# Optimization experiments

Measured on AMD Instinct MI355X. Metric: run time of the kernel, lower is better.

## Reference

```python
import jax, jax.numpy as jnp
import numpy as np
import math

D_MODEL = 1024
N_HEADS = 16
C = 1
B, L = 8, 2048


def _glorot(key, fan):
    lim = np.sqrt(6.0 / (fan + fan)).astype(np.float32)
    return jax.random.uniform(key, (fan, fan), jnp.float32, -lim, lim)


def setup_inputs() -> dict:
    key = jax.random.key(0)
    ks = jax.random.split(key, 7)
    queries = jax.random.normal(ks[0], (B, L, D_MODEL), jnp.float32)
    keys = jax.random.normal(ks[1], (B, L, D_MODEL), jnp.float32)
    values = jax.random.normal(ks[2], (B, L, D_MODEL), jnp.float32)
    wq = _glorot(ks[3], D_MODEL)
    wk = _glorot(ks[4], D_MODEL)
    wv = _glorot(ks[5], D_MODEL)
    wo = _glorot(ks[6], D_MODEL)
    return {"queries": queries, "keys": keys, "values": values,
            "wq": wq, "wk": wk, "wv": wv, "wo": wo}


def reference(queries, keys, values, wq, wk, wv, wo):
    Bv, Lv, _ = queries.shape
    H = N_HEADS
    Dh = D_MODEL // N_HEADS
    # Projections, then (B, L, H, Dh) -> (B, H, Dh, L)  (time axis last)
    Q = (queries @ wq).reshape(Bv, Lv, H, Dh).transpose(0, 2, 3, 1)
    K = (keys @ wk).reshape(Bv, Lv, H, Dh).transpose(0, 2, 3, 1)
    V = (values @ wv).reshape(Bv, Lv, H, Dh).transpose(0, 2, 3, 1)
    # FFT-based autocorrelation over the time axis, per (B,H,Dh) lane
    corr = jnp.fft.irfft(jnp.fft.rfft(Q, axis=-1) * jnp.conj(jnp.fft.rfft(K, axis=-1)), n=Lv, axis=-1)  # (B,H,Dh,L)
    k_top = int(math.floor(C * math.log(Lv)))
    top_vals, top_idx = jax.lax.top_k(corr, k_top)          # (B,H,Dh,k)
    w = jax.nn.softmax(top_vals, axis=-1)                    # (B,H,Dh,k)
    # Faithful to original roll_function: it rolls along the Dh axis
    # (which the source mislabels as seq_len), shifts taken mod Dh.
    # out[b,h,t,:] = V[b,h,(t - tau[b,h,t]) % Dh, :]
    t = jnp.arange(Dh)
    out = jnp.zeros_like(V)
    for i in range(k_top):  # small static loop (k_top = 7)
        gather_idx = (t[None, None, :] - top_idx[..., i]) % Dh   # (B,H,Dh)
        rolled = jnp.take_along_axis(V, gather_idx[..., None], axis=2)  # (B,H,Dh,L)
        out = out + w[..., i, None] * rolled
    # Faithful layout-scrambling reshape: (B,H,Dh,L)->(B,Dh,H,L)->(B,L,d_model)
    out = out.transpose(0, 2, 1, 3).reshape(Bv, Lv, D_MODEL)
    return out @ wo
```

## Files before the change

kernel.cpp:

```cpp
#include <hip/hip_runtime.h>
#include <math.h>

#define NB 8
#define NL 2048
#define ND 1024
#define NH 16
#define KTOP 7

typedef __attribute__((ext_vector_type(4))) float f32x4;
typedef __attribute__((ext_vector_type(8))) short s16x8;
typedef __attribute__((ext_vector_type(8))) _Float16 f16x8;
typedef __attribute__((ext_vector_type(4))) _Float16 f16x4;

__device__ __forceinline__ unsigned short f2bf(float x) {
  unsigned u = __float_as_uint(x);
  u = (u + 0x7FFFu + ((u >> 16) & 1u)) >> 16;
  return (unsigned short)u;
}
__device__ __forceinline__ float bf2f(unsigned short h) {
  return __uint_as_float(((unsigned)h) << 16);
}
__device__ __forceinline__ unsigned cvtpk_bf16(float a, float b) {
  unsigned d;
  asm("v_cvt_pk_bf16_f32 %0, %1, %2" : "=v"(d) : "v"(a), "v"(b));
  return d;
}
__device__ __forceinline__ float lo16(unsigned h) { return __uint_as_float(h << 16); }
__device__ __forceinline__ float hi16(unsigned h) { return __uint_as_float(h & 0xffff0000u); }

__device__ __forceinline__ void gll16(const void* g, void* l) {
  __builtin_amdgcn_global_load_lds(
      (const __attribute__((address_space(1))) void*)g,
      (__attribute__((address_space(3))) void*)l, 16, 0, 0);
}

__global__ __launch_bounds__(256) void wprep_kernel(
    const float* __restrict__ w0, const float* __restrict__ w1,
    const float* __restrict__ w2, const float* __restrict__ w3,
    short* __restrict__ wsplit, _Float16* __restrict__ wf16) {
  __shared__ float tile[32][33];
  int y = blockIdx.y;
  const float* in = (y == 0) ? w0 : (y == 1) ? w1 : (y == 2) ? w2 : w3;
  int bx = blockIdx.x & 31, by = blockIdx.x >> 5;
  int tx = threadIdx.x & 31, ty = threadIdx.x >> 5;
#pragma unroll
  for (int i = 0; i < 4; ++i)
    tile[ty + i * 8][tx] = in[(size_t)(by * 32 + ty + i * 8) * ND + bx * 32 + tx];
  __syncthreads();
#pragma unroll
  for (int i = 0; i < 4; ++i) {
    float x = tile[tx][ty + i * 8];
    int n = bx * 32 + ty + i * 8;
    int k = by * 32 + tx;
    if (y < 2) {
      short* oh = wsplit + (size_t)(2 * y) * ND * ND;
      short* ol = wsplit + (size_t)(2 * y + 1) * ND * ND;
      unsigned short h = f2bf(x);
      unsigned short l = f2bf(x - bf2f(h));
      size_t o = (size_t)n * ND + (k ^ ((n & 3) << 3));
      oh[o] = (short)h;
      ol[o] = (short)l;
    } else {
      _Float16* of = wf16 + (size_t)(y - 2) * ND * ND;
      of[(size_t)n * ND + (k ^ ((n & 7) << 3))] = (_Float16)x;
    }
  }
}

__global__ __launch_bounds__(256) void gemm_split(
    const float* __restrict__ A, const short* __restrict__ BhT,
    const short* __restrict__ BlT, float* __restrict__ Ct) {
  constexpr int K = 1024;
  __shared__ short ah[4096], al[4096], bh[4096], bl[4096];
  int t = threadIdx.x;
  int wg = (blockIdx.x & 7) * 128 + (blockIdx.x >> 3);
  int m0 = (wg >> 3) << 7, n0 = (wg & 7) << 7;
  int lane = t & 63;
  int wm = (t >> 7) & 1, wn = (t >> 6) & 1;
  int lrow = lane & 15, lk8 = (lane >> 4) << 3;

  f32x4 acc[4][4] = {};

  for (int k0 = 0; k0 < K; k0 += 32) {
#pragma unroll
    for (int it = 0; it < 2; ++it) {
      int cb = it * 256 + t;
      int r = cb >> 2, c8 = (cb & 3) << 3;
      int lo = it * 2048 + (t & 192) * 8;
      gll16(BhT + (size_t)(n0 + r) * K + k0 + c8, bh + lo);
      gll16(BlT + (size_t)(n0 + r) * K + k0 + c8, bl + lo);
    }
#pragma unroll
    for (int it = 0; it < 2; ++it) {
      int ca = it * 256 + t;
      int r = ca >> 2, c8 = (ca & 3) << 3;
      const float* pa = A + (size_t)(m0 + r) * K + k0 + c8;
      float4 x = *(const float4*)pa;
      float4 y = *(const float4*)(pa + 4);
      unsigned h0 = cvtpk_bf16(x.x, x.y);
      unsigned h1 = cvtpk_bf16(x.z, x.w);
      unsigned h2 = cvtpk_bf16(y.x, y.y);
      unsigned h3 = cvtpk_bf16(y.z, y.w);
      float r0 = x.x - lo16(h0), r1 = x.y - hi16(h0);
      float r2 = x.z - lo16(h1), r3 = x.w - hi16(h1);
      float r4 = y.x - lo16(h2), r5 = y.y - hi16(h2);
      float r6 = y.z - lo16(h3), r7 = y.w - hi16(h3);
      unsigned l0 = cvtpk_bf16(r0, r1);
      unsigned l1 = cvtpk_bf16(r2, r3);
      unsigned l2 = cvtpk_bf16(r4, r5);
      unsigned l3 = cvtpk_bf16(r6, r7);
      int wi = r * 32 + (c8 ^ ((r & 3) << 3));
      *(uint4*)(ah + wi) = make_uint4(h0, h1, h2, h3);
      *(uint4*)(al + wi) = make_uint4(l0, l1, l2, l3);
    }
    __syncthreads();

    s16x8 afh[4], afl[4];
#pragma unroll
    for (int mf = 0; mf < 4; ++mf) {
      int row = wm * 64 + mf * 16 + lrow;
      int idx = row * 32 + (lk8 ^ ((row & 3) << 3));
      afh[mf] = *(const s16x8*)(ah + idx);
      afl[mf] = *(const s16x8*)(al + idx);
    }
#pragma unroll
    for (int nf = 0; nf < 4; ++nf) {
      int row = wn * 64 + nf * 16 + lrow;
      int idx = row * 32 + (lk8 ^ ((row & 3) << 3));
      s16x8 bfh = *(const s16x8*)(bh + idx);
      s16x8 bfl = *(const s16x8*)(bl + idx);
#pragma unroll
      for (int mf = 0; mf < 4; ++mf)
        acc[mf][nf] = __builtin_amdgcn_mfma_f32_16x16x32_bf16(afh[mf], bfh, acc[mf][nf], 0, 0, 0);
#pragma unroll
      for (int mf = 0; mf < 4; ++mf)
        acc[mf][nf] = __builtin_amdgcn_mfma_f32_16x16x32_bf16(afh[mf], bfl, acc[mf][nf], 0, 0, 0);
#pragma unroll
      for (int mf = 0; mf < 4; ++mf)
        acc[mf][nf] = __builtin_amdgcn_mfma_f32_16x16x32_bf16(afl[mf], bfh, acc[mf][nf], 0, 0, 0);
    }
    __syncthreads();
  }

  int b = m0 >> 11;
  int mlbase = (m0 & 2047) + wm * 64 + (lane >> 4) * 4;
#pragma unroll
  for (int nf = 0; nf < 4; ++nf) {
    int n = n0 + wn * 64 + nf * 16 + lrow;
    float* rowp = Ct + ((size_t)(b * ND + n)) * NL + mlbase;
#pragma unroll
    for (int mf = 0; mf < 4; ++mf)
      *(float4*)(rowp + mf * 16) = *(float4*)&acc[mf][nf];
  }
}

template <int OUTMODE, bool AF32>
__global__ __launch_bounds__(256) void gemm_f16(
    const void* __restrict__ Av, const _Float16* __restrict__ BT,
    void* __restrict__ Cv) {
  constexpr int K = 1024;
  __shared__ _Float16 sA[8192];
  __shared__ _Float16 sB[8192];
  int t = threadIdx.x;
  int wg = (blockIdx.x & 7) * 128 + (blockIdx.x >> 3);
  int m0 = (wg >> 3) << 7, n0 = (wg & 7) << 7;
  int lane = t & 63;
  int wm = (t >> 7) & 1, wn = (t >> 6) & 1;
  int lrow = lane & 15, lk = (lane >> 4) << 3;

  f32x4 acc[4][4] = {};

  for (int k0 = 0; k0 < K; k0 += 64) {
#pragma unroll
    for (int it = 0; it < 4; ++it) {
      int e = it * 256 + t;
      int r = e >> 3, c8 = (e & 7) << 3;
      int lo = it * 2048 + (t & 192) * 8;
      gll16(BT + (size_t)(n0 + r) * K + k0 + c8, sB + lo);
      if (!AF32) {
        const _Float16* Af = (const _Float16*)Av;
        gll16(Af + (size_t)(m0 + r) * K + k0 + c8, sA + lo);
      }
    }
    if (AF32) {
      const float* Af = (const float*)Av;
#pragma unroll
      for (int it = 0; it < 4; ++it) {
        int ca = it * 256 + t;
        int r = ca >> 3, c8 = (ca & 7) << 3;
        const float* pa = Af + (size_t)(m0 + r) * K + k0 + c8;
        float4 x = *(const float4*)pa;
        float4 y = *(const float4*)(pa + 4);
        f16x8 o;
        o[0] = (_Float16)x.x; o[1] = (_Float16)x.y; o[2] = (_Float16)x.z; o[3] = (_Float16)x.w;
        o[4] = (_Float16)y.x; o[5] = (_Float16)y.y; o[6] = (_Float16)y.z; o[7] = (_Float16)y.w;
        *(f16x8*)(sA + r * 64 + (c8 ^ ((r & 7) << 3))) = o;
      }
    }
    __syncthreads();
#pragma unroll
    for (int kk = 0; kk < 64; kk += 32) {
      f16x8 af[4];
#pragma unroll
      for (int mf = 0; mf < 4; ++mf) {
        int row = wm * 64 + mf * 16 + lrow;
        af[mf] = *(const f16x8*)(sA + row * 64 + ((kk + lk) ^ ((row & 7) << 3)));
      }
#pragma unroll
      for (int nf = 0; nf < 4; ++nf) {
        int row = wn * 64 + nf * 16 + lrow;
        f16x8 bf = *(const f16x8*)(sB + row * 64 + ((kk + lk) ^ ((row & 7) << 3)));
#pragma unroll
        for (int mf = 0; mf < 4; ++mf)
          acc[mf][nf] = __builtin_amdgcn_mfma_f32_16x16x32_f16(af[mf], bf, acc[mf][nf], 0, 0, 0);
      }
    }
    __syncthreads();
  }

  if (OUTMODE == 0) {
    _Float16* C = (_Float16*)Cv;
    int b = m0 >> 11;
    int ml = (m0 & 2047) + wm * 64 + (lane >> 4) * 4;
#pragma unroll
    for (int nf = 0; nf < 4; ++nf) {
      int n = n0 + wn * 64 + nf * 16 + lrow;
      _Float16* row = C + ((size_t)(b * ND + n)) * NL + ml;
#pragma unroll
      for (int mf = 0; mf < 4; ++mf) {
        f16x4 v;
        v[0] = (_Float16)acc[mf][nf][0];
        v[1] = (_Float16)acc[mf][nf][1];
        v[2] = (_Float16)acc[mf][nf][2];
        v[3] = (_Float16)acc[mf][nf][3];
        *(f16x4*)(row + mf * 16) = v;
      }
    }
  } else {
    float* C = (float*)Cv;
#pragma unroll
    for (int mf = 0; mf < 4; ++mf)
#pragma unroll
      for (int nf = 0; nf < 4; ++nf) {
        int row = m0 + wm * 64 + mf * 16 + (lane >> 4) * 4;
        int col = n0 + wn * 64 + nf * 16 + lrow;
#pragma unroll
        for (int r = 0; r < 4; ++r)
          C[(size_t)(row + r) * ND + col] = acc[mf][nf][r];
      }
  }
}

__device__ __forceinline__ int SW(int i) { return i ^ ((i >> 4) & 7); }

__device__ __forceinline__ float2 cadd2(float2 a, float2 b) { return make_float2(a.x + b.x, a.y + b.y); }
__device__ __forceinline__ float2 csub2(float2 a, float2 b) { return make_float2(a.x - b.x, a.y - b.y); }
__device__ __forceinline__ float2 cmul2(float2 a, float2 b) {
  return make_float2(a.x * b.x - a.y * b.y, a.x * b.y + a.y * b.x);
}
__device__ __forceinline__ float2 cjs2(float2 a, float s) { return make_float2(-s * a.y, s * a.x); }
__device__ __forceinline__ float2 wtw(float rev) {
  return make_float2(__builtin_amdgcn_cosf(rev), __builtin_amdgcn_sinf(rev));
}

__device__ __forceinline__ void dft4(float2& b0, float2& b1, float2& b2, float2& b3, float s) {
  float2 t0 = cadd2(b0, b2), t1 = csub2(b0, b2);
  float2 t2 = cadd2(b1, b3), t3 = cjs2(csub2(b1, b3), s);
  b0 = cadd2(t0, t2);
  b1 = cadd2(t1, t3);
  b2 = csub2(t0, t2);
  b3 = csub2(t1, t3);
}

__device__ __forceinline__ void dft8(float2 a[8], float s) {
  float2 e0 = a[0], e1 = a[2], e2 = a[4], e3 = a[6];
  float2 o0 = a[1], o1 = a[3], o2 = a[5], o3 = a[7];
  dft4(e0, e1, e2, e3, s);
  dft4(o0, o1, o2, o3, s);
  const float c = 0.70710678118654752f;
  float2 w1 = make_float2(c, s * c);
  float2 w3 = make_float2(-c, s * c);
  o1 = cmul2(o1, w1);
  o2 = cjs2(o2, s);
  o3 = cmul2(o3, w3);
  a[0] = cadd2(e0, o0);
  a[4] = csub2(e0, o0);
  a[1] = cadd2(e1, o1);
  a[5] = csub2(e1, o1);
  a[2] = cadd2(e2, o2);
  a[6] = csub2(e2, o2);
  a[3] = cadd2(e3, o3);
  a[7] = csub2(e3, o3);
}

template <int LS>
__device__ __forceinline__ void pass8(const float2* __restrict__ in, float2* __restrict__ out,
                                      float s, int t) {
  float2 a[8];
  const float2* ip = in + (t ^ ((t >> 4) & 7));
#pragma unroll
  for (int r = 0; r < 8; ++r) a[r] = ip[256 * r];
  int k = t & (LS - 1);
  if (LS > 1) {
    float kf = s * (1.0f / (LS * 8)) * (float)k;
    float2 w1 = wtw(kf);
    float2 w4 = wtw(4.0f * kf);
    float2 w2 = cmul2(w1, w1);
    float2 w3 = cmul2(w2, w1);
    float2 w5 = cmul2(w4, w1);
    float2 w6 = cmul2(w4, w2);
    float2 w7 = cmul2(w4, w3);
    a[1] = cmul2(a[1], w1);
    a[2] = cmul2(a[2], w2);
    a[3] = cmul2(a[3], w3);
    a[4] = cmul2(a[4], w4);
    a[5] = cmul2(a[5], w5);
    a[6] = cmul2(a[6], w6);
    a[7] = cmul2(a[7], w7);
  }
  dft8(a, s);
  int ob = (t / LS) * (LS * 8) + k;
#pragma unroll
  for (int r = 0; r < 8; ++r) out[SW(ob + LS * r)] = a[r];
}

__global__ __launch_bounds__(256) void fft_topk_kernel(
    const float* __restrict__ Qt, const float* __restrict__ Kt,
    float* __restrict__ topw, int* __restrict__ topi) {
  __shared__ float2 X[2048];
  __shared__ float2 Y[2048];
  __shared__ float cv[2][4];
  __shared__ int ct[2][4];

  int t = threadIdx.x;
  size_t rix = blockIdx.x;
  const float* q = Qt + rix * NL;
  const float* k = Kt + rix * NL;

#pragma unroll
  for (int it = 0; it < 2; ++it) {
    int i0 = 4 * t + 1024 * it;
    float4 vq = *(const float4*)(q + i0);
    float4 vk = *(const float4*)(k + i0);
    int swb = SW(i0);
    X[swb ^ 0] = make_float2(vq.x, vk.x);
    X[swb ^ 1] = make_float2(vq.y, vk.y);
    X[swb ^ 2] = make_float2(vq.z, vk.z);
    X[swb ^ 3] = make_float2(vq.w, vk.w);
  }
  __syncthreads();

  pass8<1>(X, Y, -1.0f, t);
  __syncthreads();
  pass8<8>(Y, X, -1.0f, t);
  __syncthreads();
  pass8<64>(X, Y, -1.0f, t);
  __syncthreads();
#pragma unroll
  for (int h = 0; h < 2; ++h) {
    int b = t + 256 * h;
    float2 a[4];
    const float2* yp = Y + SW(b);
#pragma unroll
    for (int r = 0; r < 4; ++r) a[r] = yp[512 * r];
    float2 w = wtw(-(1.0f / 2048.0f) * (float)b);
    float2 w2 = cmul2(w, w);
    a[1] = cmul2(a[1], w);
    a[2] = cmul2(a[2], w2);
    a[3] = cmul2(a[3], cmul2(w2, w));
    dft4(a[0], a[1], a[2], a[3], -1.0f);
    float2* xp = X + SW(b);
#pragma unroll
    for (int r = 0; r < 4; ++r) xp[512 * r] = a[r];
  }
  __syncthreads();

#pragma unroll
  for (int it = 0; it < 8; ++it) {
    int f = t + 256 * it;
    int nf = (2048 - f) & 2047;
    float2 zf = X[SW(t) + 256 * it];
    float2 zn = X[SW(nf)];
    float a = zf.x, b2 = zf.y, c = zn.x, d = zn.y;
    float p = 0.5f * (a + c), qq = 0.5f * (b2 - d);
    float r2 = 0.5f * (b2 + d), s2 = -0.5f * (a - c);
    Y[SW(t) + 256 * it] = make_float2((p * r2 + qq * s2) * (1.0f / 2048.0f),
                                      (qq * r2 - p * s2) * (1.0f / 2048.0f));
  }
  __syncthreads();

  pass8<1>(Y, X, 1.0f, t);
  __syncthreads();
  pass8<8>(X, Y, 1.0f, t);
  __syncthreads();
  pass8<64>(Y, X, 1.0f, t);
  __syncthreads();

  float lv[8];
  int lt[8];
#pragma unroll
  for (int h = 0; h < 2; ++h) {
    int b = t + 256 * h;
    float2 a[4];
    const float2* xp = X + SW(b);
#pragma unroll
    for (int r = 0; r < 4; ++r) a[r] = xp[512 * r];
    float2 w = wtw((1.0f / 2048.0f) * (float)b);
    float2 w2 = cmul2(w, w);
    a[1] = cmul2(a[1], w);
    a[2] = cmul2(a[2], w2);
    a[3] = cmul2(a[3], cmul2(w2, w));
    dft4(a[0], a[1], a[2], a[3], 1.0f);
#pragma unroll
    for (int r = 0; r < 4; ++r) {
      lv[h * 4 + r] = a[r].x;
      lt[h * 4 + r] = b + 512 * r;
    }
  }

  int lane = t & 63, wave = t >> 6;
  float bv = lv[0];
  int bt = lt[0];
#pragma unroll
  for (int j = 1; j < 8; ++j)
    if (lv[j] > bv) { bv = lv[j]; bt = lt[j]; }

  float sel_v[KTOP];
  int sel_t[KTOP];
#pragma unroll
  for (int pass = 0; pass < KTOP; ++pass) {
    float rv = bv;
    int rt = bt;
#pragma unroll
    for (int m = 1; m < 64; m <<= 1) {
      float ov = __shfl_xor(rv, m, 64);
      int ot = __shfl_xor(rt, m, 64);
      if (ov > rv) { rv = ov; rt = ot; }
    }
    if (lane == 0) { cv[pass & 1][wave] = rv; ct[pass & 1][wave] = rt; }
    __syncthreads();
    float fv = cv[pass & 1][0];
    int ft = ct[pass & 1][0];
#pragma unroll
    for (int w = 1; w < 4; ++w) {
      float ov = cv[pass & 1][w];
      if (ov > fv) { fv = ov; ft = ct[pass & 1][w]; }
    }
    sel_v[pass] = fv;
    sel_t[pass] = ft;
    if (bt == ft) {
#pragma unroll
      for (int j = 0; j < 8; ++j)
        if (lt[j] == ft) lv[j] = -3.0e38f;
      bv = lv[0];
      bt = lt[0];
#pragma unroll
      for (int j = 1; j < 8; ++j)
        if (lv[j] > bv) { bv = lv[j]; bt = lt[j]; }
    }
  }

  if (t == 0) {
    float m = sel_v[0], ssum = 0.f, w[KTOP];
#pragma unroll
    for (int i = 0; i < KTOP; ++i) { w[i] = expf(sel_v[i] - m); ssum += w[i]; }
#pragma unroll
    for (int i = 0; i < KTOP; ++i) {
      topw[rix * KTOP + i] = w[i] / ssum;
      topi[rix * KTOP + i] = sel_t[i];
    }
  }
}

__global__ __launch_bounds__(256) void roll_kernel(
    const _Float16* __restrict__ V, const float* __restrict__ topw,
    const int* __restrict__ topi, _Float16* __restrict__ out) {
  __shared__ float vt[64][68];
  __shared__ float ws[64][8];
  __shared__ int ts[64][8];
  int blk = blockIdx.x;
  int b = blk >> 9;
  int h = (blk >> 5) & 15;
  int lc = blk & 31;
  int t = threadIdx.x;

#pragma unroll
  for (int it = 0; it < 2; ++it) {
    int e = it * 256 + t;
    int d = e >> 3, c8 = (e & 7) << 3;
    f16x8 v = *(const f16x8*)(V + ((size_t)(b * ND + h * 64 + d)) * NL + lc * 64 + c8);
#pragma unroll
    for (int j = 0; j < 8; ++j) vt[d][c8 + j] = (float)v[j];
  }
  for (int e = t; e < 64 * KTOP; e += 256) {
    int d = e / KTOP, i = e % KTOP;
    size_t rix = ((size_t)(b * 16 + h)) * 64 + d;
    ws[d][i] = topw[rix * KTOP + i];
    ts[d][i] = topi[rix * KTOP + i] & 63;
  }
  __syncthreads();

  int hi = lc >> 4;
  int c0 = (lc & 15) * 64;
#pragma unroll
  for (int it = 0; it < 16; ++it) {
    int e = it * 256 + t;
    int d = e >> 6, r = e & 63;
    float s = 0.f;
#pragma unroll
    for (int i = 0; i < KTOP; ++i) s += ws[d][i] * vt[(d - ts[d][i]) & 63][r];
    int rowp = d * 32 + h * 2 + hi;
    int col = c0 + r;
    out[((size_t)(b * NL + rowp)) * ND + (col ^ ((rowp & 7) << 3))] = (_Float16)s;
  }
}

extern "C" void kernel_launch(void* const* d_in, const int* in_sizes, int n_in,
                              void* d_out, int out_size, void* d_ws, size_t ws_size,
                              hipStream_t stream) {
  (void)in_sizes; (void)n_in; (void)out_size; (void)ws_size;
  const float* queries = (const float*)d_in[0];
  const float* keys    = (const float*)d_in[1];
  const float* values  = (const float*)d_in[2];
  const float* wq = (const float*)d_in[3];
  const float* wk = (const float*)d_in[4];
  const float* wv = (const float*)d_in[5];
  const float* wo = (const float*)d_in[6];
  float* outp = (float*)d_out;

  const size_t MB = 1024 * 1024;
  char* ws = (char*)d_ws;
  short*    wsplit = (short*)ws;
  _Float16* wf16   = (_Float16*)(ws + 8 * MB);
  float*    Qt     = (float*)(ws + 12 * MB);
  float*    Kt     = (float*)(ws + 76 * MB);
  float*    topw   = (float*)(ws + 140 * MB);
  int*      topi   = (int*)(ws + 140 * MB + (size_t)8192 * KTOP * 4);

  short* wqh = wsplit + (size_t)0 * ND * ND;
  short* wql = wsplit + (size_t)1 * ND * ND;
  short* wkh = wsplit + (size_t)2 * ND * ND;
  short* wkl = wsplit + (size_t)3 * ND * ND;
  _Float16* wv16 = wf16 + (size_t)0 * ND * ND;
  _Float16* wo16 = wf16 + (size_t)1 * ND * ND;

  _Float16* Vp = (_Float16*)Qt;
  _Float16* Xs = (_Float16*)Kt;

  wprep_kernel<<<dim3(1024, 4), 256, 0, stream>>>(wq, wk, wv, wo, wsplit, wf16);

  gemm_split<<<1024, 256, 0, stream>>>(queries, wqh, wql, Qt);
  gemm_split<<<1024, 256, 0, stream>>>(keys, wkh, wkl, Kt);

  fft_topk_kernel<<<8192, 256, 0, stream>>>(Qt, Kt, topw, topi);

  gemm_f16<0, true><<<1024, 256, 0, stream>>>(values, wv16, Vp);

  roll_kernel<<<NB * NH * 32, 256, 0, stream>>>(Vp, topw, topi, Xs);

  gemm_f16<2, false><<<1024, 256, 0, stream>>>(Xs, wo16, outp);
}
```

Before: 493.6 us.

## Double-buffer split-bf16 GEMM LDS tiles and prefetch next K slice

The split-precision projection GEMM now uses two LDS buffers. It prefetches the next K-slice of A (into registers) and B (via global_load_lds) while MFMAs run on the current slice, which cuts the loop to one barrier per iteration and hides global load latency. The LDS swizzle also changes from row&3 to (row>>1)&3, likely to reduce bank conflicts, and wprep is updated to match. LDS use doubles to 64KB per block, which may reduce occupancy.

```diff
diff --git a/kernel.cpp b/kernel.cpp
--- a/kernel.cpp
+++ b/kernel.cpp
@@ -32,6 +32,23 @@
   __builtin_amdgcn_global_load_lds(
       (const __attribute__((address_space(1))) void*)g,
       (__attribute__((address_space(3))) void*)l, 16, 0, 0);
+}
+
+__device__ __forceinline__ void asplit_write(float4 x, float4 y, short* ah, short* al, int wi) {
+  unsigned h0 = cvtpk_bf16(x.x, x.y);
+  unsigned h1 = cvtpk_bf16(x.z, x.w);
+  unsigned h2 = cvtpk_bf16(y.x, y.y);
+  unsigned h3 = cvtpk_bf16(y.z, y.w);
+  float r0 = x.x - lo16(h0), r1 = x.y - hi16(h0);
+  float r2 = x.z - lo16(h1), r3 = x.w - hi16(h1);
+  float r4 = y.x - lo16(h2), r5 = y.y - hi16(h2);
+  float r6 = y.z - lo16(h3), r7 = y.w - hi16(h3);
+  unsigned l0 = cvtpk_bf16(r0, r1);
+  unsigned l1 = cvtpk_bf16(r2, r3);
+  unsigned l2 = cvtpk_bf16(r4, r5);
+  unsigned l3 = cvtpk_bf16(r6, r7);
+  *(uint4*)(ah + wi) = make_uint4(h0, h1, h2, h3);
+  *(uint4*)(al + wi) = make_uint4(l0, l1, l2, l3);
 }
 
 __global__ __launch_bounds__(256) void wprep_kernel(
@@ -57,7 +74,7 @@
       short* ol = wsplit + (size_t)(2 * y + 1) * ND * ND;
       unsigned short h = f2bf(x);
       unsigned short l = f2bf(x - bf2f(h));
-      size_t o = (size_t)n * ND + (k ^ ((n & 3) << 3));
+      size_t o = (size_t)n * ND + (k ^ (((n >> 1) & 3) << 3));
       oh[o] = (short)h;
       ol[o] = (short)l;
     } else {
@@ -71,7 +88,7 @@
     const float* __restrict__ A, const short* __restrict__ BhT,
     const short* __restrict__ BlT, float* __restrict__ Ct) {
   constexpr int K = 1024;
-  __shared__ short ah[4096], al[4096], bh[4096], bl[4096];
+  __shared__ short smem[32768];
   int t = threadIdx.x;
   int wg = (blockIdx.x & 7) * 128 + (blockIdx.x >> 3);
   int m0 = (wg >> 3) << 7, n0 = (wg & 7) << 7;
@@ -79,56 +96,67 @@
   int wm = (t >> 7) & 1, wn = (t >> 6) & 1;
   int lrow = lane & 15, lk8 = (lane >> 4) << 3;
 
+  int r0 = t >> 2, r1 = r0 + 64;
+  int c8 = (t & 3) << 3;
+  int wi0 = r0 * 32 + (c8 ^ (((r0 >> 1) & 3) << 3));
+  int wi1 = r1 * 32 + (c8 ^ (((r1 >> 1) & 3) << 3));
+  int lo0 = (t & 192) * 8;
+  int lo1 = 2048 + (t & 192) * 8;
+
+  const float* pa0 = A + (size_t)(m0 + r0) * K + c8;
+  const float* pa1 = A + (size_t)(m0 + r1) * K + c8;
+  const short* pb0h = BhT + (size_t)(n0 + r0) * K + c8;
+  const short* pb1h = BhT + (size_t)(n0 + r1) * K + c8;
+  const short* pb0l = BlT + (size_t)(n0 + r0) * K + c8;
+  const short* pb1l = BlT + (size_t)(n0 + r1) * K + c8;
+
+  int iA[4], iB[4];
+#pragma unroll
+  for (int f = 0; f < 4; ++f) {
+    int ra = wm * 64 + f * 16 + lrow;
+    iA[f] = ra * 32 + (lk8 ^ (((ra >> 1) & 3) << 3));
+    int rb = wn * 64 + f * 16 + lrow;
+    iB[f] = rb * 32 + (lk8 ^ (((rb >> 1) & 3) << 3));
+  }
+
   f32x4 acc[4][4] = {};
 
+  float4 sx0 = *(const float4*)(pa0);
+  float4 sy0 = *(const float4*)(pa0 + 4);
+  float4 sx1 = *(const float4*)(pa1);
+  float4 sy1 = *(const float4*)(pa1 + 4);
+  gll16(pb0h, smem + 8192 + lo0);
+  gll16(pb1h, smem + 8192 + lo1);
+  gll16(pb0l, smem + 12288 + lo0);
+  gll16(pb1l, smem + 12288 + lo1);
+  asplit_write(sx0, sy0, smem, smem + 4096, wi0);
+  asplit_write(sx1, sy1, smem, smem + 4096, wi1);
+  __syncthreads();
+
   for (int k0 = 0; k0 < K; k0 += 32) {
-#pragma unroll
-    for (int it = 0; it < 2; ++it) {
-      int cb = it * 256 + t;
-      int r = cb >> 2, c8 = (cb & 3) << 3;
-      int lo = it * 2048 + (t & 192) * 8;
-      gll16(BhT + (size_t)(n0 + r) * K + k0 + c8, bh + lo);
-      gll16(BlT + (size_t)(n0 + r) * K + k0 + c8, bl + lo);
-    }
-#pragma unroll
-    for (int it = 0; it < 2; ++it) {
-      int ca = it * 256 + t;
-      int r = ca >> 2, c8 = (ca & 3) << 3;
-      const float* pa = A + (size_t)(m0 + r) * K + k0 + c8;
-      float4 x = *(const float4*)pa;
-      float4 y = *(const float4*)(pa + 4);
-      unsigned h0 = cvtpk_bf16(x.x, x.y);
-      unsigned h1 = cvtpk_bf16(x.z, x.w);
-      unsigned h2 = cvtpk_bf16(y.x, y.y);
-      unsigned h3 = cvtpk_bf16(y.z, y.w);
-      float r0 = x.x - lo16(h0), r1 = x.y - hi16(h0);
-      float r2 = x.z - lo16(h1), r3 = x.w - hi16(h1);
-      float r4 = y.x - lo16(h2), r5 = y.y - hi16(h2);
-      float r6 = y.z - lo16(h3), r7 = y.w - hi16(h3);
-      unsigned l0 = cvtpk_bf16(r0, r1);
-      unsigned l1 = cvtpk_bf16(r2, r3);
-      unsigned l2 = cvtpk_bf16(r4, r5);
-      unsigned l3 = cvtpk_bf16(r6, r7);
-      int wi = r * 32 + (c8 ^ ((r & 3) << 3));
-      *(uint4*)(ah + wi) = make_uint4(h0, h1, h2, h3);
-      *(uint4*)(al + wi) = make_uint4(l0, l1, l2, l3);
-    }
-    __syncthreads();
-
+    short* cb = smem + ((k0 >> 5) & 1) * 16384;
+    short* nb = smem + ((((k0 >> 5) & 1) ^ 1) * 16384);
+    bool more = (k0 + 32) < K;
+    if (more) {
+      sx0 = *(const float4*)(pa0 + k0 + 32);
+      sy0 = *(const float4*)(pa0 + k0 + 36);
+      sx1 = *(const float4*)(pa1 + k0 + 32);
+      sy1 = *(const float4*)(pa1 + k0 + 36);
+      gll16(pb0h + k0 + 32, nb + 8192 + lo0);
+      gll16(pb1h + k0 + 32, nb + 8192 + lo1);
+      gll16(pb0l + k0 + 32, nb + 12288 + lo0);
+      gll16(pb1l + k0 + 32, nb + 12288 + lo1);
+    }
     s16x8 afh[4], afl[4];
 #pragma unroll
     for (int mf = 0; mf < 4; ++mf) {
-      int row = wm * 64 + mf * 16 + lrow;
-      int idx = row * 32 + (lk8 ^ ((row & 3) << 3));
-      afh[mf] = *(const s16x8*)(ah + idx);
-      afl[mf] = *(const s16x8*)(al + idx);
+      afh[mf] = *(const s16x8*)(cb + iA[mf]);
+      afl[mf] = *(const s16x8*)(cb + 4096 + iA[mf]);
     }
 #pragma unroll
     for (int nf = 0; nf < 4; ++nf) {
-      int row = wn * 64 + nf * 16 + lrow;
-      int idx = row * 32 + (lk8 ^ ((row & 3) << 3));
-      s16x8 bfh = *(const s16x8*)(bh + idx);
-      s16x8 bfl = *(const s16x8*)(bl + idx);
+      s16x8 bfh = *(const s16x8*)(cb + 8192 + iB[nf]);
+      s16x8 bfl = *(const s16x8*)(cb + 12288 + iB[nf]);
 #pragma unroll
       for (int mf = 0; mf < 4; ++mf)
         acc[mf][nf] = __builtin_amdgcn_mfma_f32_16x16x32_bf16(afh[mf], bfh, acc[mf][nf], 0, 0, 0);
@@ -138,6 +166,10 @@
 #pragma unroll
       for (int mf = 0; mf < 4; ++mf)
         acc[mf][nf] = __builtin_amdgcn_mfma_f32_16x16x32_bf16(afl[mf], bfh, acc[mf][nf], 0, 0, 0);
+    }
+    if (more) {
+      asplit_write(sx0, sy0, nb, nb + 4096, wi0);
+      asplit_write(sx1, sy1, nb, nb + 4096, wi1);
     }
     __syncthreads();
   }
```

Result: faster. 467.1 us (-5.4%).

## Double-buffer B tiles and load A fragments directly into registers in split GEMM

Applied to the files above, without the earlier changes.

The split-bf16 GEMM now double-buffers the B (weight) tiles in LDS, prefetching the next K-slice while computing the current one. The A operand is no longer staged through LDS: each wave loads its own fp32 rows from global memory and converts them to hi/lo bf16 fragments in registers. The weight swizzle pattern and launch bounds change to match the new layout. This removes one barrier per iteration and the A LDS traffic, at the cost of redundant global A loads across the two wn waves and more register pressure.

```diff
diff --git a/kernel.cpp b/kernel.cpp
--- a/kernel.cpp
+++ b/kernel.cpp
@@ -9,6 +9,7 @@
 
 typedef __attribute__((ext_vector_type(4))) float f32x4;
 typedef __attribute__((ext_vector_type(8))) short s16x8;
+typedef __attribute__((ext_vector_type(4))) unsigned u32x4;
 typedef __attribute__((ext_vector_type(8))) _Float16 f16x8;
 typedef __attribute__((ext_vector_type(4))) _Float16 f16x4;
 
@@ -57,7 +58,7 @@
       short* ol = wsplit + (size_t)(2 * y + 1) * ND * ND;
       unsigned short h = f2bf(x);
       unsigned short l = f2bf(x - bf2f(h));
-      size_t o = (size_t)n * ND + (k ^ ((n & 3) << 3));
+      size_t o = (size_t)n * ND + (k ^ (((n >> 1) & 3) << 3));
       oh[o] = (short)h;
       ol[o] = (short)l;
     } else {
@@ -67,11 +68,11 @@
   }
 }
 
-__global__ __launch_bounds__(256) void gemm_split(
+__global__ __launch_bounds__(256, 3) void gemm_split(
     const float* __restrict__ A, const short* __restrict__ BhT,
     const short* __restrict__ BlT, float* __restrict__ Ct) {
   constexpr int K = 1024;
-  __shared__ short ah[4096], al[4096], bh[4096], bl[4096];
+  __shared__ short smem[16384];
   int t = threadIdx.x;
   int wg = (blockIdx.x & 7) * 128 + (blockIdx.x >> 3);
   int m0 = (wg >> 3) << 7, n0 = (wg & 7) << 7;
@@ -79,24 +80,49 @@
   int wm = (t >> 7) & 1, wn = (t >> 6) & 1;
   int lrow = lane & 15, lk8 = (lane >> 4) << 3;
 
+  int rb0 = t >> 2, rb1 = rb0 + 64;
+  int c8 = (t & 3) << 3;
+  int lo0 = (t & 192) * 8;
+  int lo1 = 2048 + (t & 192) * 8;
+  const short* pb0h = BhT + (size_t)(n0 + rb0) * K + c8;
+  const short* pb1h = BhT + (size_t)(n0 + rb1) * K + c8;
+  const short* pb0l = BlT + (size_t)(n0 + rb0) * K + c8;
+  const short* pb1l = BlT + (size_t)(n0 + rb1) * K + c8;
+
+  const float* pA[4];
+#pragma unroll
+  for (int mf = 0; mf < 4; ++mf)
+    pA[mf] = A + (size_t)(m0 + wm * 64 + mf * 16 + lrow) * K + lk8;
+
+  int iB[4];
+#pragma unroll
+  for (int f = 0; f < 4; ++f) {
+    int rb = wn * 64 + f * 16 + lrow;
+    iB[f] = rb * 32 + (lk8 ^ (((rb >> 1) & 3) << 3));
+  }
+
   f32x4 acc[4][4] = {};
 
+  gll16(pb0h, smem + lo0);
+  gll16(pb1h, smem + lo1);
+  gll16(pb0l, smem + 4096 + lo0);
+  gll16(pb1l, smem + 4096 + lo1);
+  __syncthreads();
+
   for (int k0 = 0; k0 < K; k0 += 32) {
-#pragma unroll
-    for (int it = 0; it < 2; ++it) {
-      int cb = it * 256 + t;
-      int r = cb >> 2, c8 = (cb & 3) << 3;
-      int lo = it * 2048 + (t & 192) * 8;
-      gll16(BhT + (size_t)(n0 + r) * K + k0 + c8, bh + lo);
-      gll16(BlT + (size_t)(n0 + r) * K + k0 + c8, bl + lo);
-    }
-#pragma unroll
-    for (int it = 0; it < 2; ++it) {
-      int ca = it * 256 + t;
-      int r = ca >> 2, c8 = (ca & 3) << 3;
-      const float* pa = A + (size_t)(m0 + r) * K + k0 + c8;
-      float4 x = *(const float4*)pa;
-      float4 y = *(const float4*)(pa + 4);
+    short* cb = smem + ((k0 >> 5) & 1) * 8192;
+    short* nb = smem + ((((k0 >> 5) & 1) ^ 1) * 8192);
+    if (k0 + 32 < K) {
+      gll16(pb0h + k0 + 32, nb + lo0);
+      gll16(pb1h + k0 + 32, nb + lo1);
+      gll16(pb0l + k0 + 32, nb + 4096 + lo0);
+      gll16(pb1l + k0 + 32, nb + 4096 + lo1);
+    }
+    s16x8 afh[4], afl[4];
+#pragma unroll
+    for (int mf = 0; mf < 4; ++mf) {
+      float4 x = *(const float4*)(pA[mf] + k0);
+      float4 y = *(const float4*)(pA[mf] + k0 + 4);
       unsigned h0 = cvtpk_bf16(x.x, x.y);
       unsigned h1 = cvtpk_bf16(x.z, x.w);
       unsigned h2 = cvtpk_bf16(y.x, y.y);
@@ -105,30 +131,16 @@
       float r2 = x.z - lo16(h1), r3 = x.w - hi16(h1);
       float r4 = y.x - lo16(h2), r5 = y.y - hi16(h2);
       float r6 = y.z - lo16(h3), r7 = y.w - hi16(h3);
-      unsigned l0 = cvtpk_bf16(r0, r1);
-      unsigned l1 = cvtpk_bf16(r2, r3);
-      unsigned l2 = cvtpk_bf16(r4, r5);
-      unsigned l3 = cvtpk_bf16(r6, r7);
-      int wi = r * 32 + (c8 ^ ((r & 3) << 3));
-      *(uint4*)(ah + wi) = make_uint4(h0, h1, h2, h3);
-      *(uint4*)(al + wi) = make_uint4(l0, l1, l2, l3);
-    }
-    __syncthreads();
-
-    s16x8 afh[4], afl[4];
-#pragma unroll
-    for (int mf = 0; mf < 4; ++mf) {
-      int row = wm * 64 + mf * 16 + lrow;
-      int idx = row * 32 + (lk8 ^ ((row & 3) << 3));
-      afh[mf] = *(const s16x8*)(ah + idx);
-      afl[mf] = *(const s16x8*)(al + idx);
+      u32x4 hv = {h0, h1, h2, h3};
+      u32x4 lv = {cvtpk_bf16(r0, r1), cvtpk_bf16(r2, r3),
+                  cvtpk_bf16(r4, r5), cvtpk_bf16(r6, r7)};
+      afh[mf] = __builtin_bit_cast(s16x8, hv);
+      afl[mf] = __builtin_bit_cast(s16x8, lv);
     }
 #pragma unroll
     for (int nf = 0; nf < 4; ++nf) {
-      int row = wn * 64 + nf * 16 + lrow;
-      int idx = row * 32 + (lk8 ^ ((row & 3) << 3));
-      s16x8 bfh = *(const s16x8*)(bh + idx);
-      s16x8 bfl = *(const s16x8*)(bl + idx);
+      s16x8 bfh = *(const s16x8*)(cb + iB[nf]);
+      s16x8 bfl = *(const s16x8*)(cb + 4096 + iB[nf]);
 #pragma unroll
       for (int mf = 0; mf < 4; ++mf)
         acc[mf][nf] = __builtin_amdgcn_mfma_f32_16x16x32_bf16(afh[mf], bfh, acc[mf][nf], 0, 0, 0);
```

Result: slower. 634.8 us (+28.6%).
